# Performance work log

Hardware: AMD Instinct MI355X
Metric: run time of the kernel (lower is better)

## Reference

```python
import jax, jax.numpy as jnp
import numpy as np

E, TOPK = 8, 2
N_EMBD, TEXT_DIM, FULL = 1024, 1024, 1024
BS, SEQ = 8, 512

def setup_inputs() -> dict:
    key = jax.random.key(0)
    ks = jax.random.split(key, 8)
    return {
        "x": jax.random.normal(ks[0], (BS, SEQ, N_EMBD), jnp.float32),
        "dec_embeddings": jax.random.normal(ks[1], (BS, TEXT_DIM), jnp.float32),
        # router is zero-init in the module, but use small random weights so top-k is non-degenerate
        "router_w": jax.random.normal(ks[2], (E, TEXT_DIM), jnp.float32) * 0.02,
        "router_b": jnp.zeros((E,), jnp.float32),
        "w1": jax.random.normal(ks[3], (E, N_EMBD, N_EMBD), jnp.float32) * 0.02,
        "w2": jax.random.normal(ks[4], (E, N_EMBD, FULL), jnp.float32) * 0.02,
        "b1": jnp.zeros((E, 1, N_EMBD), jnp.float32),
        "b2": jnp.zeros((E, 1, FULL), jnp.float32),
    }

def reference(x, dec_embeddings, router_w, router_b, w1, w2, b1, b2):
    bs, seqlen, n_embd = x.shape
    logits = dec_embeddings @ router_w.T + router_b          # (bs, E)
    gate_probs = jax.nn.softmax(logits, axis=-1)
    topk_w, topk_idx = jax.lax.top_k(gate_probs, TOPK)       # (bs, k)
    topk_w = topk_w / jnp.sum(topk_w, axis=-1, keepdims=True)
    # dense all-expert 2-layer MLP (as written in the original)
    hidden = jax.nn.relu(jnp.einsum('bsn,enh->ebsh', x, w1) + b1[:, None])   # (E,bs,S,H)
    out_all = jnp.einsum('ebsh,ehf->ebsf', hidden, w2) + b2[:, None]          # (E,bs,S,F)
    out_b = jnp.transpose(out_all, (1, 0, 2, 3))             # (bs,E,S,F)
    # gather top-k expert outputs per batch item and combine
    sel = jnp.take_along_axis(out_b, topk_idx[:, :, None, None], axis=1)      # (bs,k,S,F)
    final_output = jnp.sum(topk_w[:, :, None, None] * sel, axis=1)            # (bs,S,F)
    combined_mask = jnp.max(jax.nn.one_hot(topk_idx, E, dtype=x.dtype), axis=1)  # (bs,E)
    aux_loss = E * jnp.sum(jnp.mean(gate_probs, axis=0) * jnp.mean(combined_mask, axis=0))
    return final_output, aux_loss, combined_mask, logits
```

## Files before the change

kernel.cpp:

```cpp
#include <hip/hip_runtime.h>
#include <hip/hip_bf16.h>
#include <stdint.h>

#define EXP 8
#define DIM 1024
#define SEQL 512
#define BATCH 8
#define OFF_AUX    4194304
#define OFF_MASK   4194305
#define OFF_LOGITS 4194369

typedef __bf16 bf16_t;
typedef bf16_t bf16x8 __attribute__((ext_vector_type(8)));
typedef bf16_t bf16x4 __attribute__((ext_vector_type(4)));
typedef float  f32x4  __attribute__((ext_vector_type(4)));

typedef __attribute__((address_space(1))) void* as1p;
typedef __attribute__((address_space(3))) void* as3p;

__device__ __forceinline__ void glds16(const void* g, void* l) {
  __builtin_amdgcn_global_load_lds((as1p)(void*)g, (as3p)l, 16, 0, 0);
}

__global__ __launch_bounds__(256) void prep_kernel(
    const float* __restrict__ x, const float* __restrict__ dec,
    const float* __restrict__ rw, const float* __restrict__ rb,
    const float* __restrict__ w1, const float* __restrict__ w2,
    bf16_t* __restrict__ xb, bf16_t* __restrict__ w1t, bf16_t* __restrict__ w2t,
    float* __restrict__ out_aux, float* __restrict__ out_mask,
    float* __restrict__ out_logits, int* __restrict__ idx_ws,
    float* __restrict__ w_ws) {
  __shared__ __align__(16) char smem[64 * 68 * 4];
  const int bid = blockIdx.x;
  const int t = threadIdx.x;

  if (bid < 4096) {
    const int z = bid >> 8;
    const int rem = bid & 255;
    const int k0 = (rem >> 4) * 64, n0 = (rem & 15) * 64;
    const float* src = (z < 8) ? (w1 + (size_t)z * DIM * DIM)
                               : (w2 + (size_t)(z - 8) * DIM * DIM);
    bf16_t* dst = (z < 8) ? (w1t + (size_t)z * DIM * DIM)
                          : (w2t + (size_t)(z - 8) * DIM * DIM);
    float (*tile)[68] = (float (*)[68])smem;
    const int r = t >> 4, c = t & 15;
    float4 v[4];
#pragma unroll
    for (int i = 0; i < 4; ++i)
      v[i] = *(const float4*)(src + (size_t)(k0 + r + 16 * i) * DIM + n0 + c * 4);
#pragma unroll
    for (int i = 0; i < 4; ++i)
      *(float4*)&tile[r + 16 * i][c * 4] = v[i];
    __syncthreads();
#pragma unroll
    for (int i2 = 0; i2 < 2; ++i2) {
      const int n = t & 63, kc = (t >> 6) + 4 * i2;
      bf16x8 o;
#pragma unroll
      for (int wd = 0; wd < 8; ++wd) o[wd] = (bf16_t)tile[kc * 8 + wd][n];
      *(bf16x8*)(dst + (size_t)(n0 + n) * DIM + k0 + kc * 8) = o;
    }
  } else if (bid < 4096 + 512) {
    const int i0 = (bid - 4096) * 2048 + t;
    float4 v[8];
#pragma unroll
    for (int i = 0; i < 8; ++i) v[i] = ((const float4*)x)[i0 + i * 256];
#pragma unroll
    for (int i = 0; i < 8; ++i) {
      bf16x4 o;
      o[0] = (bf16_t)v[i].x; o[1] = (bf16_t)v[i].y;
      o[2] = (bf16_t)v[i].z; o[3] = (bf16_t)v[i].w;
      ((bf16x4*)xb)[i0 + i * 256] = o;
    }
  } else {
    float* part  = (float*)smem;
    float* lg64  = part + 256;
    float* probs = lg64 + 64;
    float* msk   = probs + 64;
    const int p = t >> 2, seg = t & 3;
    const int b = p >> 3, e = p & 7;
    const float4* dv = (const float4*)(dec + b * DIM + seg * 256);
    const float4* wv = (const float4*)(rw + e * DIM + seg * 256);
    float s = 0.f;
#pragma unroll 8
    for (int i = 0; i < 64; ++i) {
      float4 a = dv[i], c = wv[i];
      s += a.x * c.x + a.y * c.y + a.z * c.z + a.w * c.w;
    }
    part[t] = s;
    __syncthreads();
    if (seg == 0) {
      float l = part[t] + part[t + 1] + part[t + 2] + part[t + 3] + rb[e];
      lg64[p] = l;
      out_logits[p] = l;
    }
    __syncthreads();
    if (t < 8) {
      float l[8];
      float mx = -1e30f;
#pragma unroll
      for (int k = 0; k < 8; ++k) { l[k] = lg64[t * 8 + k]; mx = fmaxf(mx, l[k]); }
      float pe[8];
      float sum = 0.f;
#pragma unroll
      for (int k = 0; k < 8; ++k) { pe[k] = expf(l[k] - mx); sum += pe[k]; }
      float inv = 1.f / sum;
#pragma unroll
      for (int k = 0; k < 8; ++k) { pe[k] *= inv; probs[t * 8 + k] = pe[k]; }
      int i0 = 0;
#pragma unroll
      for (int k = 1; k < 8; ++k) if (pe[k] > pe[i0]) i0 = k;
      int i1 = (i0 == 0) ? 1 : 0;
#pragma unroll
      for (int k = 0; k < 8; ++k) if (k != i0 && pe[k] > pe[i1]) i1 = k;
      float p0 = pe[i0], p1 = pe[i1];
      float invs = 1.f / (p0 + p1);
      idx_ws[t * 2] = i0;
      idx_ws[t * 2 + 1] = i1;
      w_ws[t * 2] = p0 * invs;
      w_ws[t * 2 + 1] = p1 * invs;
#pragma unroll
      for (int k = 0; k < 8; ++k) {
        float m = (k == i0 || k == i1) ? 1.f : 0.f;
        msk[t * 8 + k] = m;
        out_mask[t * 8 + k] = m;
      }
    }
    __syncthreads();
    if (t == 0) {
      float aux = 0.f;
#pragma unroll
      for (int k = 0; k < 8; ++k) {
        float mp = 0.f, mm = 0.f;
#pragma unroll
        for (int bb = 0; bb < 8; ++bb) { mp += probs[bb * 8 + k]; mm += msk[bb * 8 + k]; }
        aux += (mp * 0.125f) * (mm * 0.125f);
      }
      out_aux[0] = 8.f * aux;
    }
  }
}

__device__ __forceinline__ void kloop512(const bf16_t* __restrict__ A,
                                         const bf16_t* __restrict__ Bt,
                                         char* sA, char* sB, int t,
                                         f32x4 acc[4][2]) {
  const int lane = t & 63;
  const int w = t >> 6;
  const int wm = w & 1, wn = w >> 1;
  const int m15 = lane & 15, q = lane >> 4;
  const int rl = t >> 2, cp = (t & 3) ^ (rl & 3);
  const bf16_t* ga = A  + (size_t)rl * DIM + cp * 8;
  const bf16_t* gb = Bt + (size_t)rl * DIM + cp * 8;

  const char* ra[4];
  const char* rb[2];
#pragma unroll
  for (int i = 0; i < 4; ++i) {
    const int r = wm * 64 + i * 16 + m15;
    ra[i] = sA + r * 64 + ((q ^ (r & 3)) * 16);
  }
#pragma unroll
  for (int j = 0; j < 2; ++j) {
    const int n = wn * 32 + j * 16 + m15;
    rb[j] = sB + n * 64 + ((q ^ (n & 3)) * 16);
  }

  glds16(ga, sA + t * 16);
  glds16(gb, sB + t * 16);

  for (int kt = 0; kt < 32; ++kt) {
    const int cur = kt & 1;
    __syncthreads();
    if (kt < 31) {
      const int nxt = cur ^ 1;
      const int off = (kt + 1) * 32;
      glds16(ga + off, sA + nxt * 8192 + t * 16);
      glds16(gb + off, sB + nxt * 8192 + t * 16);
    }
    bf16x8 af[4], bfr[2];
#pragma unroll
    for (int i = 0; i < 4; ++i) af[i] = *(const bf16x8*)(ra[i] + cur * 8192);
#pragma unroll
    for (int j = 0; j < 2; ++j) bfr[j] = *(const bf16x8*)(rb[j] + cur * 8192);
#pragma unroll
    for (int i = 0; i < 4; ++i)
#pragma unroll
      for (int j = 0; j < 2; ++j)
        acc[i][j] = __builtin_amdgcn_mfma_f32_16x16x32_bf16(af[i], bfr[j], acc[i][j], 0, 0, 0);
  }
}

__global__ __launch_bounds__(512, 4) void gemm1_kernel(
    const bf16_t* __restrict__ xb, const bf16_t* __restrict__ w1t,
    const float* __restrict__ b1, const float* __restrict__ b2,
    const int* __restrict__ topk_idx, const float* __restrict__ topk_w,
    bf16_t* __restrict__ hidden, float* __restrict__ out) {
  __shared__ __align__(16) char smem[32768];
  const int tid = threadIdx.x;
  const int bN = blockIdx.x, bM = blockIdx.y, slot = blockIdx.z;

  if (slot == 16) {
    const int b = bN;
    const int s0 = bM * 128;
    const float g0 = topk_w[b * 2], g1 = topk_w[b * 2 + 1];
    const float4* be0 = (const float4*)(b2 + topk_idx[b * 2] * DIM);
    const float4* be1 = (const float4*)(b2 + topk_idx[b * 2 + 1] * DIM);
    const int f4 = tid & 255, rr = tid >> 8;
    const float4 v0 = be0[f4], v1 = be1[f4];
    float4 bb;
    bb.x = g0 * v0.x + g1 * v1.x;
    bb.y = g0 * v0.y + g1 * v1.y;
    bb.z = g0 * v0.z + g1 * v1.z;
    bb.w = g0 * v0.w + g1 * v1.w;
    float* O = out + (size_t)b * SEQL * DIM;
#pragma unroll
    for (int k = 0; k < 64; ++k)
      *(float4*)(O + (size_t)(s0 + rr + 2 * k) * DIM + f4 * 4) = bb;
    return;
  }

  const int b = slot >> 1;
  const int e = topk_idx[slot];
  const float gw = topk_w[slot];

  const bf16_t* A  = xb + ((size_t)b * SEQL + bM * 128) * DIM;
  const bf16_t* Bt = w1t + ((size_t)e * DIM + bN * 128) * DIM;

  f32x4 acc[4][2];
#pragma unroll
  for (int i = 0; i < 4; ++i)
#pragma unroll
    for (int j = 0; j < 2; ++j) acc[i][j] = {0.f, 0.f, 0.f, 0.f};

  kloop512(A, Bt, smem, smem + 16384, tid, acc);

  const int lane = tid & 63, w = tid >> 6;
  const int wm = w & 1, wn = w >> 1;
  const int m15 = lane & 15, q = lane >> 4;
  const float* be = b1 + e * DIM;
  bf16_t* hb = (bf16_t*)smem;
  bf16_t* H = hidden + (size_t)slot * SEQL * DIM + ((size_t)bM * 128) * DIM + bN * 128;
#pragma unroll
  for (int h = 0; h < 2; ++h) {
    __syncthreads();
    if (wm == h) {
#pragma unroll
      for (int i = 0; i < 4; ++i)
#pragma unroll
        for (int j = 0; j < 2; ++j) {
          const int colL = wn * 32 + j * 16 + m15;
          const float bias = be[bN * 128 + colL];
#pragma unroll
          for (int r = 0; r < 4; ++r) {
            const int lr = i * 16 + q * 4 + r;
            hb[lr * 136 + colL] = (bf16_t)(gw * fmaxf(acc[i][j][r] + bias, 0.f));
          }
        }
    }
    __syncthreads();
#pragma unroll
    for (int ii = 0; ii < 2; ++ii) {
      const int c2 = tid + 512 * ii;
      const int r = c2 >> 4, c = c2 & 15;
      bf16x8 vv = *(const bf16x8*)(hb + r * 136 + c * 8);
      *(bf16x8*)(H + (size_t)(h * 64 + r) * DIM + c * 8) = vv;
    }
  }
}

__global__ __launch_bounds__(512, 4) void gemm2_kernel(
    const bf16_t* __restrict__ hidden, const bf16_t* __restrict__ w2t,
    const int* __restrict__ topk_idx, float* __restrict__ out) {
  __shared__ __align__(16) char smem[32768];
  const int tid = threadIdx.x;
  const int bN = blockIdx.x, bM = blockIdx.y, slot = blockIdx.z;
  const int b = slot >> 1;
  const int e = topk_idx[slot];

  const bf16_t* A  = hidden + ((size_t)slot * SEQL + bM * 128) * DIM;
  const bf16_t* Bt = w2t + ((size_t)e * DIM + bN * 128) * DIM;

  f32x4 acc[4][2];
#pragma unroll
  for (int i = 0; i < 4; ++i)
#pragma unroll
    for (int j = 0; j < 2; ++j) acc[i][j] = {0.f, 0.f, 0.f, 0.f};

  kloop512(A, Bt, smem, smem + 16384, tid, acc);

  const int lane = tid & 63, w = tid >> 6;
  const int wm = w & 1, wn = w >> 1;
  const int m15 = lane & 15, q = lane >> 4;
  float* O = out + (size_t)b * SEQL * DIM;
#pragma unroll
  for (int i = 0; i < 4; ++i) {
    const int row = bM * 128 + wm * 64 + i * 16 + q * 4;
#pragma unroll
    for (int j = 0; j < 2; ++j) {
      const int col = bN * 128 + wn * 32 + j * 16 + m15;
#pragma unroll
      for (int r = 0; r < 4; ++r)
        atomicAdd(&O[(size_t)(row + r) * DIM + col], acc[i][j][r]);
    }
  }
}

extern "C" void kernel_launch(void* const* d_in, const int* in_sizes, int n_in,
                              void* d_out, int out_size, void* d_ws, size_t ws_size,
                              hipStream_t stream) {
  const float* x   = (const float*)d_in[0];
  const float* dec = (const float*)d_in[1];
  const float* rw  = (const float*)d_in[2];
  const float* rb  = (const float*)d_in[3];
  const float* w1  = (const float*)d_in[4];
  const float* w2  = (const float*)d_in[5];
  const float* b1  = (const float*)d_in[6];
  const float* b2  = (const float*)d_in[7];
  float* out = (float*)d_out;

  char* ws = (char*)d_ws;
  bf16_t* xb   = (bf16_t*)(ws);
  bf16_t* w1t  = (bf16_t*)(ws + (8u << 20));
  bf16_t* w2t  = (bf16_t*)(ws + (24u << 20));
  bf16_t* hid  = (bf16_t*)(ws + (40u << 20));
  int*    idxw = (int*)(ws + (56u << 20));
  float*  ww   = (float*)(ws + (56u << 20) + 64);

  hipLaunchKernelGGL(prep_kernel, dim3(4096 + 512 + 1), dim3(256), 0, stream,
                     x, dec, rw, rb, w1, w2, xb, w1t, w2t,
                     out + OFF_AUX, out + OFF_MASK, out + OFF_LOGITS, idxw, ww);
  hipLaunchKernelGGL(gemm1_kernel, dim3(8, 4, 17), dim3(512), 0, stream,
                     xb, w1t, b1, b2, idxw, ww, hid, out);
  hipLaunchKernelGGL(gemm2_kernel, dim3(8, 4, 16), dim3(512), 0, stream,
                     hid, w2t, idxw, out);
}
```

Measured before the change: 219.7 us.

## Give each wave a private LDS tile pipeline and drop block barriers in GEMMs

The block-shared double-buffered K loop with __syncthreads is replaced by per-wave private LDS buffers. Each wave loads its own 64x64 A and B tiles with global_load_lds and synchronises only through manual s_waitcnt, prefetching two k-steps ahead. Blocks shrink from 512 to 256 threads, each wave computes a 64x64 output tile (4x4 MFMA accumulators), and LDS per block doubles to 64KB. This removes block-wide barriers but drops A/B tile sharing across waves, which raises global/L2 traffic and register pressure, and it relies on hand-coded waitcnt values being correct.

```diff
diff --git a/kernel.cpp b/kernel.cpp
--- a/kernel.cpp
+++ b/kernel.cpp
@@ -21,6 +21,11 @@
 __device__ __forceinline__ void glds16(const void* g, void* l) {
   __builtin_amdgcn_global_load_lds((as1p)(void*)g, (as3p)l, 16, 0, 0);
 }
+
+#define CFENCE() asm volatile("" ::: "memory")
+#define WAIT_VM8()  { CFENCE(); __builtin_amdgcn_s_waitcnt(0x0F78); CFENCE(); }
+#define WAIT_VM0()  { CFENCE(); __builtin_amdgcn_s_waitcnt(0x0F70); CFENCE(); }
+#define WAIT_LGKM() { CFENCE(); __builtin_amdgcn_s_waitcnt(0xC07F); CFENCE(); }
 
 __global__ __launch_bounds__(256) void prep_kernel(
     const float* __restrict__ x, const float* __restrict__ dec,
@@ -141,62 +146,94 @@
   }
 }
 
-__device__ __forceinline__ void kloop512(const bf16_t* __restrict__ A,
-                                         const bf16_t* __restrict__ Bt,
-                                         char* sA, char* sB, int t,
-                                         f32x4 acc[4][2]) {
-  const int lane = t & 63;
-  const int w = t >> 6;
-  const int wm = w & 1, wn = w >> 1;
+__device__ __forceinline__ void kloop_wave(const bf16_t* __restrict__ A,
+                                           const bf16_t* __restrict__ Bt,
+                                           char* wlds, int lane,
+                                           f32x4 acc[4][4]) {
   const int m15 = lane & 15, q = lane >> 4;
-  const int rl = t >> 2, cp = (t & 3) ^ (rl & 3);
-  const bf16_t* ga = A  + (size_t)rl * DIM + cp * 8;
-  const bf16_t* gb = Bt + (size_t)rl * DIM + cp * 8;
-
-  const char* ra[4];
-  const char* rb[2];
+  const int srow = lane >> 2;
+  const int scp  = (lane & 3) ^ ((lane >> 3) & 3);
+  const bf16_t* gA[4];
+  const bf16_t* gB[4];
 #pragma unroll
   for (int i = 0; i < 4; ++i) {
-    const int r = wm * 64 + i * 16 + m15;
-    ra[i] = sA + r * 64 + ((q ^ (r & 3)) * 16);
-  }
-#pragma unroll
-  for (int j = 0; j < 2; ++j) {
-    const int n = wn * 32 + j * 16 + m15;
-    rb[j] = sB + n * 64 + ((q ^ (n & 3)) * 16);
-  }
-
-  glds16(ga, sA + t * 16);
-  glds16(gb, sB + t * 16);
-
-  for (int kt = 0; kt < 32; ++kt) {
-    const int cur = kt & 1;
-    __syncthreads();
-    if (kt < 31) {
-      const int nxt = cur ^ 1;
-      const int off = (kt + 1) * 32;
-      glds16(ga + off, sA + nxt * 8192 + t * 16);
-      glds16(gb + off, sB + nxt * 8192 + t * 16);
-    }
-    bf16x8 af[4], bfr[2];
-#pragma unroll
-    for (int i = 0; i < 4; ++i) af[i] = *(const bf16x8*)(ra[i] + cur * 8192);
-#pragma unroll
-    for (int j = 0; j < 2; ++j) bfr[j] = *(const bf16x8*)(rb[j] + cur * 8192);
-#pragma unroll
-    for (int i = 0; i < 4; ++i)
-#pragma unroll
-      for (int j = 0; j < 2; ++j)
+    gA[i] = A  + (size_t)(i * 16 + srow) * DIM + scp * 8;
+    gB[i] = Bt + (size_t)(i * 16 + srow) * DIM + scp * 8;
+  }
+  char* lA = wlds;
+  char* lB = wlds + 8192;
+  const int sw = (q ^ ((m15 >> 1) & 3)) * 16;
+  int off_[4];
+#pragma unroll
+  for (int i = 0; i < 4; ++i) off_[i] = (i * 16 + m15) * 64 + sw;
+
+#pragma unroll
+  for (int i = 0; i < 4; ++i) {
+    glds16(gA[i], lA + i * 1024 + lane * 16);
+    glds16(gB[i], lB + i * 1024 + lane * 16);
+  }
+#pragma unroll
+  for (int i = 0; i < 4; ++i) {
+    glds16(gA[i] + 32, lA + 4096 + i * 1024 + lane * 16);
+    glds16(gB[i] + 32, lB + 4096 + i * 1024 + lane * 16);
+  }
+
+#pragma unroll 2
+  for (int kt = 0; kt < 30; ++kt) {
+    const int buf = (kt & 1) * 4096;
+    WAIT_VM8();
+    bf16x8 af[4], bfr[4];
+#pragma unroll
+    for (int i = 0; i < 4; ++i) af[i]  = *(const bf16x8*)(lA + buf + off_[i]);
+#pragma unroll
+    for (int j = 0; j < 4; ++j) bfr[j] = *(const bf16x8*)(lB + buf + off_[j]);
+    WAIT_LGKM();
+    const int go = (kt + 2) * 32;
+#pragma unroll
+    for (int i = 0; i < 4; ++i) {
+      glds16(gA[i] + go, lA + buf + i * 1024 + lane * 16);
+      glds16(gB[i] + go, lB + buf + i * 1024 + lane * 16);
+    }
+#pragma unroll
+    for (int i = 0; i < 4; ++i)
+#pragma unroll
+      for (int j = 0; j < 4; ++j)
         acc[i][j] = __builtin_amdgcn_mfma_f32_16x16x32_bf16(af[i], bfr[j], acc[i][j], 0, 0, 0);
   }
-}
-
-__global__ __launch_bounds__(512, 4) void gemm1_kernel(
+  {
+    WAIT_VM8();
+    bf16x8 af[4], bfr[4];
+#pragma unroll
+    for (int i = 0; i < 4; ++i) af[i]  = *(const bf16x8*)(lA + off_[i]);
+#pragma unroll
+    for (int j = 0; j < 4; ++j) bfr[j] = *(const bf16x8*)(lB + off_[j]);
+#pragma unroll
+    for (int i = 0; i < 4; ++i)
+#pragma unroll
+      for (int j = 0; j < 4; ++j)
+        acc[i][j] = __builtin_amdgcn_mfma_f32_16x16x32_bf16(af[i], bfr[j], acc[i][j], 0, 0, 0);
+  }
+  {
+    WAIT_VM0();
+    bf16x8 af[4], bfr[4];
+#pragma unroll
+    for (int i = 0; i < 4; ++i) af[i]  = *(const bf16x8*)(lA + 4096 + off_[i]);
+#pragma unroll
+    for (int j = 0; j < 4; ++j) bfr[j] = *(const bf16x8*)(lB + 4096 + off_[j]);
+#pragma unroll
+    for (int i = 0; i < 4; ++i)
+#pragma unroll
+      for (int j = 0; j < 4; ++j)
+        acc[i][j] = __builtin_amdgcn_mfma_f32_16x16x32_bf16(af[i], bfr[j], acc[i][j], 0, 0, 0);
+  }
+}
+
+__global__ __launch_bounds__(256, 2) void gemm1_kernel(
     const bf16_t* __restrict__ xb, const bf16_t* __restrict__ w1t,
     const float* __restrict__ b1, const float* __restrict__ b2,
     const int* __restrict__ topk_idx, const float* __restrict__ topk_w,
     bf16_t* __restrict__ hidden, float* __restrict__ out) {
-  __shared__ __align__(16) char smem[32768];
+  __shared__ __align__(16) char smem[65536];
   const int tid = threadIdx.x;
   const int bN = blockIdx.x, bM = blockIdx.y, slot = blockIdx.z;
 
@@ -204,101 +241,93 @@
     const int b = bN;
     const int s0 = bM * 128;
     const float g0 = topk_w[b * 2], g1 = topk_w[b * 2 + 1];
-    const float4* be0 = (const float4*)(b2 + topk_idx[b * 2] * DIM);
-    const float4* be1 = (const float4*)(b2 + topk_idx[b * 2 + 1] * DIM);
-    const int f4 = tid & 255, rr = tid >> 8;
-    const float4 v0 = be0[f4], v1 = be1[f4];
+    const float4 v0 = ((const float4*)(b2 + topk_idx[b * 2] * DIM))[tid];
+    const float4 v1 = ((const float4*)(b2 + topk_idx[b * 2 + 1] * DIM))[tid];
     float4 bb;
     bb.x = g0 * v0.x + g1 * v1.x;
     bb.y = g0 * v0.y + g1 * v1.y;
     bb.z = g0 * v0.z + g1 * v1.z;
     bb.w = g0 * v0.w + g1 * v1.w;
     float* O = out + (size_t)b * SEQL * DIM;
-#pragma unroll
-    for (int k = 0; k < 64; ++k)
-      *(float4*)(O + (size_t)(s0 + rr + 2 * k) * DIM + f4 * 4) = bb;
+#pragma unroll 8
+    for (int row = 0; row < 128; ++row)
+      *(float4*)(O + (size_t)(s0 + row) * DIM + tid * 4) = bb;
     return;
   }
 
+  const int lane = tid & 63, w = tid >> 6;
+  const int wm = w & 1, wn = w >> 1;
+  char* wlds = smem + w * 16384;
   const int b = slot >> 1;
   const int e = topk_idx[slot];
   const float gw = topk_w[slot];
 
-  const bf16_t* A  = xb + ((size_t)b * SEQL + bM * 128) * DIM;
-  const bf16_t* Bt = w1t + ((size_t)e * DIM + bN * 128) * DIM;
-
-  f32x4 acc[4][2];
+  const bf16_t* A  = xb + ((size_t)b * SEQL + bM * 128 + wm * 64) * DIM;
+  const bf16_t* Bt = w1t + ((size_t)e * DIM + bN * 128 + wn * 64) * DIM;
+
+  f32x4 acc[4][4];
 #pragma unroll
   for (int i = 0; i < 4; ++i)
 #pragma unroll
-    for (int j = 0; j < 2; ++j) acc[i][j] = {0.f, 0.f, 0.f, 0.f};
-
-  kloop512(A, Bt, smem, smem + 16384, tid, acc);
-
+    for (int j = 0; j < 4; ++j) acc[i][j] = {0.f, 0.f, 0.f, 0.f};
+
+  kloop_wave(A, Bt, wlds, lane, acc);
+
+  const int m15 = lane & 15, q = lane >> 4;
+  const float* be = b1 + e * DIM + bN * 128 + wn * 64;
+  bf16_t* hb = (bf16_t*)wlds;
+#pragma unroll
+  for (int j = 0; j < 4; ++j) {
+    const float bias = be[j * 16 + m15];
+#pragma unroll
+    for (int i = 0; i < 4; ++i)
+#pragma unroll
+      for (int r = 0; r < 4; ++r)
+        hb[(i * 16 + q * 4 + r) * 72 + j * 16 + m15] =
+            (bf16_t)(gw * fmaxf(acc[i][j][r] + bias, 0.f));
+  }
+  CFENCE();
+  bf16_t* H = hidden + (size_t)slot * SEQL * DIM +
+              ((size_t)(bM * 128 + wm * 64)) * DIM + bN * 128 + wn * 64;
+#pragma unroll
+  for (int it = 0; it < 8; ++it) {
+    const int idx = it * 64 + lane;
+    const int row = idx >> 3, ch = idx & 7;
+    *(bf16x8*)(H + (size_t)row * DIM + ch * 8) = *(const bf16x8*)(hb + row * 72 + ch * 8);
+  }
+}
+
+__global__ __launch_bounds__(256, 2) void gemm2_kernel(
+    const bf16_t* __restrict__ hidden, const bf16_t* __restrict__ w2t,
+    const int* __restrict__ topk_idx, float* __restrict__ out) {
+  __shared__ __align__(16) char smem[65536];
+  const int tid = threadIdx.x;
+  const int bN = blockIdx.x, bM = blockIdx.y, slot = blockIdx.z;
   const int lane = tid & 63, w = tid >> 6;
   const int wm = w & 1, wn = w >> 1;
-  const int m15 = lane & 15, q = lane >> 4;
-  const float* be = b1 + e * DIM;
-  bf16_t* hb = (bf16_t*)smem;
-  bf16_t* H = hidden + (size_t)slot * SEQL * DIM + ((size_t)bM * 128) * DIM + bN * 128;
-#pragma unroll
-  for (int h = 0; h < 2; ++h) {
-    __syncthreads();
-    if (wm == h) {
-#pragma unroll
-      for (int i = 0; i < 4; ++i)
-#pragma unroll
-        for (int j = 0; j < 2; ++j) {
-          const int colL = wn * 32 + j * 16 + m15;
-          const float bias = be[bN * 128 + colL];
-#pragma unroll
-          for (int r = 0; r < 4; ++r) {
-            const int lr = i * 16 + q * 4 + r;
-            hb[lr * 136 + colL] = (bf16_t)(gw * fmaxf(acc[i][j][r] + bias, 0.f));
-          }
-        }
-    }
-    __syncthreads();
-#pragma unroll
-    for (int ii = 0; ii < 2; ++ii) {
-      const int c2 = tid + 512 * ii;
-      const int r = c2 >> 4, c = c2 & 15;
-      bf16x8 vv = *(const bf16x8*)(hb + r * 136 + c * 8);
-      *(bf16x8*)(H + (size_t)(h * 64 + r) * DIM + c * 8) = vv;
-    }
-  }
-}
-
-__global__ __launch_bounds__(512, 4) void gemm2_kernel(
-    const bf16_t* __restrict__ hidden, const bf16_t* __restrict__ w2t,
-    const int* __restrict__ topk_idx, float* __restrict__ out) {
-  __shared__ __align__(16) char smem[32768];
-  const int tid = threadIdx.x;
-  const int bN = blockIdx.x, bM = blockIdx.y, slot = blockIdx.z;
+  char* wlds = smem + w * 16384;
   const int b = slot >> 1;
   const int e = topk_idx[slot];
 
-  const bf16_t* A  = hidden + ((size_t)slot * SEQL + bM * 128) * DIM;
-  const bf16_t* Bt = w2t + ((size_t)e * DIM + bN * 128) * DIM;
-
-  f32x4 acc[4][2];
+  const bf16_t* A  = hidden + ((size_t)slot * SEQL + bM * 128 + wm * 64) * DIM;
+  const bf16_t* Bt = w2t + ((size_t)e * DIM + bN * 128 + wn * 64) * DIM;
+
+  f32x4 acc[4][4];
 #pragma unroll
   for (int i = 0; i < 4; ++i)
 #pragma unroll
-    for (int j = 0; j < 2; ++j) acc[i][j] = {0.f, 0.f, 0.f, 0.f};
-
-  kloop512(A, Bt, smem, smem + 16384, tid, acc);
-
-  const int lane = tid & 63, w = tid >> 6;
-  const int wm = w & 1, wn = w >> 1;
+    for (int j = 0; j < 4; ++j) acc[i][j] = {0.f, 0.f, 0.f, 0.f};
+
+  kloop_wave(A, Bt, wlds, lane, acc);
+
   const int m15 = lane & 15, q = lane >> 4;
   float* O = out + (size_t)b * SEQL * DIM;
 #pragma unroll
   for (int i = 0; i < 4; ++i) {
     const int row = bM * 128 + wm * 64 + i * 16 + q * 4;
 #pragma unroll
-    for (int j = 0; j < 2; ++j) {
-      const int col = bN * 128 + wn * 32 + j * 16 + m15;
+    for (int j = 0; j < 4; ++j) {
+      const int col = bN * 128 + wn * 64 + j * 16 + m15;
 #pragma unroll
       for (int r = 0; r < 4; ++r)
         atomicAdd(&O[(size_t)(row + r) * DIM + col], acc[i][j][r]);
@@ -330,8 +359,8 @@
   hipLaunchKernelGGL(prep_kernel, dim3(4096 + 512 + 1), dim3(256), 0, stream,
                      x, dec, rw, rb, w1, w2, xb, w1t, w2t,
                      out + OFF_AUX, out + OFF_MASK, out + OFF_LOGITS, idxw, ww);
-  hipLaunchKernelGGL(gemm1_kernel, dim3(8, 4, 17), dim3(512), 0, stream,
+  hipLaunchKernelGGL(gemm1_kernel, dim3(8, 4, 17), dim3(256), 0, stream,
                      xb, w1t, b1, b2, idxw, ww, hid, out);
-  hipLaunchKernelGGL(gemm2_kernel, dim3(8, 4, 16), dim3(512), 0, stream,
+  hipLaunchKernelGGL(gemm2_kernel, dim3(8, 4, 16), dim3(256), 0, stream,
                      hid, w2t, idxw, out);
 }
```

Result: slower. 253.9 us (+15.5%).
